# Performance work log

Hardware: AMD Instinct MI355X
Metric: run time of the kernel (lower is better)

The kernel has to match this reference:

```python
import jax, jax.numpy as jnp
import numpy as np

N_EMBD = 1024
NUM_EXPERTS = 8
TOP_K = 2


def new_gelu(x):
    # NewGELU: tanh approximation used by GPT-2
    c = jnp.sqrt(2.0 / jnp.pi).astype(x.dtype)
    return 0.5 * x * (1.0 + jnp.tanh(c * (x + 0.044715 * x ** 3)))


def setup_inputs() -> dict:
    key = jax.random.key(0)
    ks = jax.random.split(key, 6)
    C, E, H = N_EMBD, NUM_EXPERTS, 4 * N_EMBD
    x = jax.random.normal(ks[0], (4, 2048, C), dtype=jnp.float32)
    router_w = 0.02 * jax.random.normal(ks[1], (E, C), dtype=jnp.float32)  # Linear(C,E,bias=False).weight
    w1 = 0.02 * jax.random.normal(ks[2], (E, H, C), dtype=jnp.float32)     # c_fc.weight per expert
    b1 = jnp.zeros((E, H), dtype=jnp.float32)
    w2 = 0.02 * jax.random.normal(ks[3], (E, C, H), dtype=jnp.float32)     # c_proj.weight per expert
    b2 = jnp.zeros((E, C), dtype=jnp.float32)
    return {"x": x, "router_w": router_w, "w1": w1, "b1": b1, "w2": w2, "b2": b2}


def reference(x, router_w, w1, b1, w2, b2):
    B, T, C = x.shape
    E = router_w.shape[0]
    x_flat = x.reshape(B * T, C)  # [N, C]

    router_logits = x_flat @ router_w.T              # [N, E]
    router_probs = jax.nn.softmax(router_logits, axis=-1)
    top_k_probs, top_k_idx = jax.lax.top_k(router_probs, TOP_K)  # [N, K]
    top_k_probs = top_k_probs / (top_k_probs.sum(axis=-1, keepdims=True) + 1e-8)

    # combine weights per (token, expert): sum over k of gate_k * onehot(idx_k)
    cw = (jax.nn.one_hot(top_k_idx, E, dtype=x.dtype) * top_k_probs[..., None]).sum(axis=1)  # [N, E]

    output = jnp.zeros_like(x_flat)
    for e in range(E):  # small fixed expert count
        h = new_gelu(x_flat @ w1[e].T + b1[e])       # [N, 4C]
        out_e = h @ w2[e].T + b2[e]                  # [N, C]
        output = output + cw[:, e:e + 1] * out_e

    return output.reshape(B, T, C)
```

## Files before the change

### kernel.cpp

```cpp
#include <hip/hip_runtime.h>
#include <hip/hip_bf16.h>
#include <math.h>


#define N_TOK   8192
#define C_DIM   1024
#define H_DIM   4096
#define N_EXP   8
#define CAP     8192

typedef __bf16 bf16;
typedef bf16  bf16x8 __attribute__((ext_vector_type(8)));
typedef float f32x4  __attribute__((ext_vector_type(4)));

__device__ __forceinline__ void async_ld16(const void* g, void* l) {
    __builtin_amdgcn_global_load_lds(
        (const __attribute__((address_space(1))) void*)g,
        (__attribute__((address_space(3))) void*)l,
        16, 0, 0);
}

__device__ __forceinline__ float gelu_f(float v) {
    float u = v + 0.044715f * v * v * v;
    return 0.5f * v * (1.0f + tanhf(0.7978845608028654f * u));
}

__global__ void cvt_k(const float* __restrict__ src, bf16* __restrict__ dst, int n8) {
    int i = blockIdx.x * blockDim.x + threadIdx.x;
    if (i >= n8) return;
    const float4* p = (const float4*)src + (size_t)i * 2;
    float4 a = p[0], b = p[1];
    bf16x8 v;
    v[0] = (bf16)a.x; v[1] = (bf16)a.y; v[2] = (bf16)a.z; v[3] = (bf16)a.w;
    v[4] = (bf16)b.x; v[5] = (bf16)b.y; v[6] = (bf16)b.z; v[7] = (bf16)b.w;
    *((bf16x8*)dst + i) = v;
}

__global__ __launch_bounds__(1024) void router_k(const float* __restrict__ x,
                                                 const float* __restrict__ rw,
                                                 int* __restrict__ counts,
                                                 int* __restrict__ tok,
                                                 float* __restrict__ gate) {
    __shared__ int lcnt[N_EXP];
    __shared__ int lbase[N_EXP];
    const int tid  = threadIdx.x;
    const int lane = tid & 63;
    const int wv   = tid >> 6;
    if (tid < N_EXP) lcnt[tid] = 0;
    __syncthreads();

    const int t = blockIdx.x * 16 + wv;

    float dot[N_EXP];
#pragma unroll
    for (int e = 0; e < N_EXP; ++e) dot[e] = 0.f;
    const float4* xr = (const float4*)(x + (size_t)t * C_DIM);
#pragma unroll
    for (int j = 0; j < 4; ++j) {
        float4 xv = xr[j * 64 + lane];
#pragma unroll
        for (int e = 0; e < N_EXP; ++e) {
            float4 w4 = ((const float4*)(rw + (size_t)e * C_DIM))[j * 64 + lane];
            dot[e] += xv.x * w4.x + xv.y * w4.y + xv.z * w4.z + xv.w * w4.w;
        }
    }
#pragma unroll
    for (int e = 0; e < N_EXP; ++e) {
#pragma unroll
        for (int o = 32; o > 0; o >>= 1) dot[e] += __shfl_xor(dot[e], o, 64);
    }

    int a = 0, b = 0, ra = 0, rb = 0;
    float g0 = 0.f, g1 = 0.f;
    if (lane == 0) {
        float m = dot[0];
#pragma unroll
        for (int e = 1; e < N_EXP; ++e) m = fmaxf(m, dot[e]);
        float p[N_EXP]; float s = 0.f;
#pragma unroll
        for (int e = 0; e < N_EXP; ++e) { p[e] = expf(dot[e] - m); s += p[e]; }
        a = 0;
#pragma unroll
        for (int e = 1; e < N_EXP; ++e) if (p[e] > p[a]) a = e;
        b = -1;
#pragma unroll
        for (int e = 0; e < N_EXP; ++e) if (e != a && (b < 0 || p[e] > p[b])) b = e;
        float pa = p[a] / s, pb = p[b] / s;
        float d = pa + pb + 1e-8f;
        g0 = pa / d; g1 = pb / d;
        ra = atomicAdd(&lcnt[a], 1);
        rb = atomicAdd(&lcnt[b], 1);
    }
    __syncthreads();
    if (tid < N_EXP) lbase[tid] = atomicAdd(&counts[tid], lcnt[tid]);
    __syncthreads();
    if (lane == 0) {
        int sa = lbase[a] + ra;
        int sb = lbase[b] + rb;
        tok[a * CAP + sa] = t;  gate[a * CAP + sa] = g0;
        tok[b * CAP + sb] = t;  gate[b * CAP + sb] = g1;
    }
}

__global__ void prefix_k(const int* __restrict__ counts, int* __restrict__ offs) {
    if (threadIdx.x == 0) {
        int s = 0;
        for (int e = 0; e < N_EXP; ++e) { offs[e] = s; s += counts[e]; }
    }
}


__global__ __launch_bounds__(256) void fc1_k(const bf16* __restrict__ xb,
                                             const bf16* __restrict__ w1b,
                                             const float* __restrict__ b1,
                                             const int* __restrict__ counts,
                                             const int* __restrict__ offs,
                                             const int* __restrict__ tok,
                                             bf16* __restrict__ h) {
    const int e   = blockIdx.z;
    const int cnt = counts[e];
    const int m0  = blockIdx.y * 128;
    if (m0 >= cnt) return;
    const int n0  = blockIdx.x * 128;
    const int off = offs[e];

    __shared__ __align__(16) bf16 As[128][32];
    __shared__ __align__(16) bf16 Bs[128][32];

    const int tid  = threadIdx.x;
    const int lane = tid & 63;
    const int wv   = tid >> 6;
    const int wm   = wv & 1;
    const int wn   = wv >> 1;

    const int scol = (((lane & 3) ^ ((lane >> 3) & 3))) * 8;

    const int ar0 = wv * 16 + (lane >> 2);
    const int ar1 = 64 + wv * 16 + (lane >> 2);
    const int i0 = m0 + ar0, i1 = m0 + ar1;
    const int t0 = tok[e * CAP + (i0 < cnt ? i0 : cnt - 1)];
    const int t1 = tok[e * CAP + (i1 < cnt ? i1 : cnt - 1)];
    const bf16* ga0 = xb + (size_t)t0 * C_DIM + scol;
    const bf16* ga1 = xb + (size_t)t1 * C_DIM + scol;
    bf16* la0 = &As[wv * 16][0];
    bf16* la1 = &As[64 + wv * 16][0];

    const bf16* gb0 = w1b + ((size_t)e * H_DIM + n0 + ar0) * C_DIM + scol;
    const bf16* gb1 = w1b + ((size_t)e * H_DIM + n0 + ar1) * C_DIM + scol;
    bf16* lb0 = &Bs[wv * 16][0];
    bf16* lb1 = &Bs[64 + wv * 16][0];

    f32x4 acc[4][4];
#pragma unroll
    for (int mi = 0; mi < 4; ++mi)
#pragma unroll
        for (int ni = 0; ni < 4; ++ni)
#pragma unroll
            for (int r = 0; r < 4; ++r) acc[mi][ni][r] = 0.f;

    const int r_   = lane & 15;
    const int g_   = lane >> 4;
    const int rcol = (g_ ^ ((r_ >> 1) & 3)) * 8;

    for (int kt = 0; kt < C_DIM / 32; ++kt) {
        const int k0 = kt * 32;
        async_ld16(ga0 + k0, la0);
        async_ld16(ga1 + k0, la1);
        async_ld16(gb0 + k0, lb0);
        async_ld16(gb1 + k0, lb1);
        __syncthreads();

        bf16x8 af[4];
#pragma unroll
        for (int mi = 0; mi < 4; ++mi)
            af[mi] = *(const bf16x8*)&As[wm * 64 + mi * 16 + r_][rcol];
#pragma unroll
        for (int ni = 0; ni < 4; ++ni) {
            bf16x8 bfr = *(const bf16x8*)&Bs[wn * 64 + ni * 16 + r_][rcol];
#pragma unroll
            for (int mi = 0; mi < 4; ++mi)
                acc[mi][ni] = __builtin_amdgcn_mfma_f32_16x16x32_bf16(af[mi], bfr, acc[mi][ni], 0, 0, 0);
        }
        __syncthreads();
    }

    const int lg = lane >> 4, ln = lane & 15;
#pragma unroll
    for (int mi = 0; mi < 4; ++mi) {
#pragma unroll
        for (int r = 0; r < 4; ++r) {
            const int m = wm * 64 + mi * 16 + lg * 4 + r;
            if (m0 + m < cnt) {
                const size_t hrow = (size_t)(off + m0 + m) * H_DIM;
#pragma unroll
                for (int ni = 0; ni < 4; ++ni) {
                    const int n = n0 + wn * 64 + ni * 16 + ln;
                    float v = acc[mi][ni][r] + b1[(size_t)e * H_DIM + n];
                    h[hrow + n] = (bf16)gelu_f(v);
                }
            }
        }
    }
}

__global__ __launch_bounds__(256) void fc2_k(const bf16* __restrict__ h,
                                             const bf16* __restrict__ w2b,
                                             const float* __restrict__ b2,
                                             const int* __restrict__ counts,
                                             const int* __restrict__ offs,
                                             const int* __restrict__ tok,
                                             const float* __restrict__ gate,
                                             float* __restrict__ out) {
    const int e   = blockIdx.z;
    const int cnt = counts[e];
    const int m0  = blockIdx.y * 128;
    if (m0 >= cnt) return;
    const int n0  = blockIdx.x * 128;
    const int off = offs[e];

    __shared__ __align__(16) bf16 As[128][32];
    __shared__ __align__(16) bf16 Bs[128][32];

    const int tid  = threadIdx.x;
    const int lane = tid & 63;
    const int wv   = tid >> 6;
    const int wm   = wv & 1;
    const int wn   = wv >> 1;

    const int scol = (((lane & 3) ^ ((lane >> 3) & 3))) * 8;

    const int ar0 = wv * 16 + (lane >> 2);
    const int ar1 = 64 + wv * 16 + (lane >> 2);
    const int i0 = m0 + ar0, i1 = m0 + ar1;
    const size_t hr0 = (size_t)(off + (i0 < cnt ? i0 : cnt - 1)) * H_DIM;
    const size_t hr1 = (size_t)(off + (i1 < cnt ? i1 : cnt - 1)) * H_DIM;
    const bf16* ga0 = h + hr0 + scol;
    const bf16* ga1 = h + hr1 + scol;
    bf16* la0 = &As[wv * 16][0];
    bf16* la1 = &As[64 + wv * 16][0];

    const bf16* gb0 = w2b + ((size_t)e * C_DIM + n0 + ar0) * H_DIM + scol;
    const bf16* gb1 = w2b + ((size_t)e * C_DIM + n0 + ar1) * H_DIM + scol;
    bf16* lb0 = &Bs[wv * 16][0];
    bf16* lb1 = &Bs[64 + wv * 16][0];

    f32x4 acc[4][4];
#pragma unroll
    for (int mi = 0; mi < 4; ++mi)
#pragma unroll
        for (int ni = 0; ni < 4; ++ni)
#pragma unroll
            for (int r = 0; r < 4; ++r) acc[mi][ni][r] = 0.f;

    const int r_   = lane & 15;
    const int g_   = lane >> 4;
    const int rcol = (g_ ^ ((r_ >> 1) & 3)) * 8;

    for (int kt = 0; kt < H_DIM / 32; ++kt) {
        const int k0 = kt * 32;
        async_ld16(ga0 + k0, la0);
        async_ld16(ga1 + k0, la1);
        async_ld16(gb0 + k0, lb0);
        async_ld16(gb1 + k0, lb1);
        __syncthreads();

        bf16x8 af[4];
#pragma unroll
        for (int mi = 0; mi < 4; ++mi)
            af[mi] = *(const bf16x8*)&As[wm * 64 + mi * 16 + r_][rcol];
#pragma unroll
        for (int ni = 0; ni < 4; ++ni) {
            bf16x8 bfr = *(const bf16x8*)&Bs[wn * 64 + ni * 16 + r_][rcol];
#pragma unroll
            for (int mi = 0; mi < 4; ++mi)
                acc[mi][ni] = __builtin_amdgcn_mfma_f32_16x16x32_bf16(af[mi], bfr, acc[mi][ni], 0, 0, 0);
        }
        __syncthreads();
    }

    const int lg = lane >> 4, ln = lane & 15;
#pragma unroll
    for (int mi = 0; mi < 4; ++mi) {
#pragma unroll
        for (int r = 0; r < 4; ++r) {
            const int m = wm * 64 + mi * 16 + lg * 4 + r;
            if (m0 + m < cnt) {
                const int   tk = tok[e * CAP + m0 + m];
                const float g  = gate[e * CAP + m0 + m];
#pragma unroll
                for (int ni = 0; ni < 4; ++ni) {
                    const int n = n0 + wn * 64 + ni * 16 + ln;
                    float v = (acc[mi][ni][r] + b2[(size_t)e * C_DIM + n]) * g;
                    atomicAdd(&out[(size_t)tk * C_DIM + n], v);
                }
            }
        }
    }
}

extern "C" void kernel_launch(void* const* d_in, const int* in_sizes, int n_in,
                              void* d_out, int out_size, void* d_ws, size_t ws_size,
                              hipStream_t stream) {
    const float* x  = (const float*)d_in[0];
    const float* rw = (const float*)d_in[1];
    const float* w1 = (const float*)d_in[2];
    const float* b1 = (const float*)d_in[3];
    const float* w2 = (const float*)d_in[4];
    const float* b2 = (const float*)d_in[5];
    float* out = (float*)d_out;

    char* ws = (char*)d_ws;
    size_t o = 0;
    bf16* xb     = (bf16*)(ws + o);  o += (size_t)N_TOK * C_DIM * sizeof(bf16);
    bf16* w1b    = (bf16*)(ws + o);  o += (size_t)N_EXP * H_DIM * C_DIM * sizeof(bf16);
    bf16* w2b    = (bf16*)(ws + o);  o += (size_t)N_EXP * C_DIM * H_DIM * sizeof(bf16);
    int*  tok    = (int*)(ws + o);   o += (size_t)N_EXP * CAP * sizeof(int);
    float* gate  = (float*)(ws + o); o += (size_t)N_EXP * CAP * sizeof(float);
    int*  counts = (int*)(ws + o);   o += 128;
    int*  offs   = (int*)(ws + o);   o += 128;
    bf16* h      = (bf16*)(ws + o);  o += (size_t)(2 * N_TOK) * H_DIM * sizeof(bf16);

    hipMemsetAsync(d_out, 0, (size_t)N_TOK * C_DIM * sizeof(float), stream);
    hipMemsetAsync(counts, 0, 128, stream);

    const int NW = N_EXP * H_DIM * C_DIM / 8;
    cvt_k<<<dim3((N_TOK * C_DIM / 8 + 255) / 256), 256, 0, stream>>>(x, xb, N_TOK * C_DIM / 8);
    cvt_k<<<dim3((NW + 255) / 256), 256, 0, stream>>>(w1, w1b, NW);
    cvt_k<<<dim3((NW + 255) / 256), 256, 0, stream>>>(w2, w2b, NW);
    router_k<<<dim3(N_TOK / 16), dim3(1024), 0, stream>>>(x, rw, counts, tok, gate);
    prefix_k<<<dim3(1), dim3(64), 0, stream>>>(counts, offs);
    fc1_k<<<dim3(H_DIM / 128, N_TOK / 128, N_EXP), dim3(256), 0, stream>>>(xb, w1b, b1, counts, offs, tok, h);
    fc2_k<<<dim3(C_DIM / 128, N_TOK / 128, N_EXP), dim3(256), 0, stream>>>(h, w2b, b2, counts, offs, tok, gate, out);
}
```

Before: 908.2 us.

## Double-buffer GEMM LDS tiles, remap blocks per XCD, fuse conversions, drop prefix kernel

The fc1 and fc2 GEMM loops now double-buffer the LDS tiles, issuing the async global-to-LDS loads for the next K-step before the MFMAs on the current one, so load latency overlaps compute. Block indices are remapped so consecutive hardware block IDs, which are spread round-robin across the 8 XCDs, map to the same expert's tiles on one XCD, aiming to improve L2 reuse of weights. The three fp32-to-bf16 conversion launches are merged into one kernel, and the prefix-sum kernel is removed by having each GEMM block add up the preceding expert counts itself. Double-buffering doubles LDS per block. Because there is only one barrier per iteration, the next stage's async writes may race with reads of the buffer being overwritten, so it relies on the completion ordering of the async loads.

```diff
diff --git a/kernel.cpp b/kernel.cpp
--- a/kernel.cpp
+++ b/kernel.cpp
@@ -25,15 +25,28 @@
     return 0.5f * v * (1.0f + tanhf(0.7978845608028654f * u));
 }
 
-__global__ void cvt_k(const float* __restrict__ src, bf16* __restrict__ dst, int n8) {
-    int i = blockIdx.x * blockDim.x + threadIdx.x;
-    if (i >= n8) return;
-    const float4* p = (const float4*)src + (size_t)i * 2;
+#define NX8 ((size_t)N_TOK * C_DIM / 8)
+#define NW8 ((size_t)N_EXP * H_DIM * C_DIM / 8)
+#define NCVT (NX8 + 2 * NW8)
+
+__global__ __launch_bounds__(256) void cvt_all_k(const float* __restrict__ x,
+                                                 const float* __restrict__ w1,
+                                                 const float* __restrict__ w2,
+                                                 bf16* __restrict__ xb,
+                                                 bf16* __restrict__ w1b,
+                                                 bf16* __restrict__ w2b) {
+    size_t i = (size_t)blockIdx.x * 256 + threadIdx.x;
+    if (i >= NCVT) return;
+    const float* src; bf16* dst; size_t j;
+    if (i < NX8)            { src = x;  dst = xb;  j = i; }
+    else if (i < NX8 + NW8) { src = w1; dst = w1b; j = i - NX8; }
+    else                    { src = w2; dst = w2b; j = i - NX8 - NW8; }
+    const float4* p = (const float4*)src + j * 2;
     float4 a = p[0], b = p[1];
     bf16x8 v;
     v[0] = (bf16)a.x; v[1] = (bf16)a.y; v[2] = (bf16)a.z; v[3] = (bf16)a.w;
     v[4] = (bf16)b.x; v[5] = (bf16)b.y; v[6] = (bf16)b.z; v[7] = (bf16)b.w;
-    *((bf16x8*)dst + i) = v;
+    *((bf16x8*)dst + j) = v;
 }
 
 __global__ __launch_bounds__(1024) void router_k(const float* __restrict__ x,
@@ -102,30 +115,29 @@
     }
 }
 
-__global__ void prefix_k(const int* __restrict__ counts, int* __restrict__ offs) {
-    if (threadIdx.x == 0) {
-        int s = 0;
-        for (int e = 0; e < N_EXP; ++e) { offs[e] = s; s += counts[e]; }
-    }
-}
-
 
 __global__ __launch_bounds__(256) void fc1_k(const bf16* __restrict__ xb,
                                              const bf16* __restrict__ w1b,
                                              const float* __restrict__ b1,
                                              const int* __restrict__ counts,
-                                             const int* __restrict__ offs,
                                              const int* __restrict__ tok,
                                              bf16* __restrict__ h) {
-    const int e   = blockIdx.z;
+    const int lin = blockIdx.x + 32 * (blockIdx.y + 64 * blockIdx.z);
+    const int w   = (lin & 7) * 2048 + (lin >> 3);
+    const int e   = w >> 11;
+    const int by  = (w >> 5) & 63;
+    const int bx  = w & 31;
+
     const int cnt = counts[e];
-    const int m0  = blockIdx.y * 128;
+    const int m0  = by * 128;
     if (m0 >= cnt) return;
-    const int n0  = blockIdx.x * 128;
-    const int off = offs[e];
-
-    __shared__ __align__(16) bf16 As[128][32];
-    __shared__ __align__(16) bf16 Bs[128][32];
+    const int n0  = bx * 128;
+
+    int off = 0;
+    for (int j = 0; j < e; ++j) off += counts[j];
+
+    __shared__ __align__(16) bf16 As[2][128][32];
+    __shared__ __align__(16) bf16 Bs[2][128][32];
 
     const int tid  = threadIdx.x;
     const int lane = tid & 63;
@@ -136,19 +148,14 @@
     const int scol = (((lane & 3) ^ ((lane >> 3) & 3))) * 8;
 
     const int ar0 = wv * 16 + (lane >> 2);
-    const int ar1 = 64 + wv * 16 + (lane >> 2);
+    const int ar1 = 64 + ar0;
     const int i0 = m0 + ar0, i1 = m0 + ar1;
     const int t0 = tok[e * CAP + (i0 < cnt ? i0 : cnt - 1)];
     const int t1 = tok[e * CAP + (i1 < cnt ? i1 : cnt - 1)];
     const bf16* ga0 = xb + (size_t)t0 * C_DIM + scol;
     const bf16* ga1 = xb + (size_t)t1 * C_DIM + scol;
-    bf16* la0 = &As[wv * 16][0];
-    bf16* la1 = &As[64 + wv * 16][0];
-
     const bf16* gb0 = w1b + ((size_t)e * H_DIM + n0 + ar0) * C_DIM + scol;
     const bf16* gb1 = w1b + ((size_t)e * H_DIM + n0 + ar1) * C_DIM + scol;
-    bf16* lb0 = &Bs[wv * 16][0];
-    bf16* lb1 = &Bs[64 + wv * 16][0];
 
     f32x4 acc[4][4];
 #pragma unroll
@@ -162,27 +169,33 @@
     const int g_   = lane >> 4;
     const int rcol = (g_ ^ ((r_ >> 1) & 3)) * 8;
 
+#define STAGE1(b, kt) do { const int k0_ = (kt) * 32;        \
+    async_ld16(ga0 + k0_, &As[b][wv * 16][0]);               \
+    async_ld16(ga1 + k0_, &As[b][64 + wv * 16][0]);          \
+    async_ld16(gb0 + k0_, &Bs[b][wv * 16][0]);               \
+    async_ld16(gb1 + k0_, &Bs[b][64 + wv * 16][0]); } while (0)
+
+    STAGE1(0, 0);
+    __syncthreads();
+    int cur = 0;
     for (int kt = 0; kt < C_DIM / 32; ++kt) {
-        const int k0 = kt * 32;
-        async_ld16(ga0 + k0, la0);
-        async_ld16(ga1 + k0, la1);
-        async_ld16(gb0 + k0, lb0);
-        async_ld16(gb1 + k0, lb1);
-        __syncthreads();
+        if (kt + 1 < C_DIM / 32) STAGE1(cur ^ 1, kt + 1);
 
         bf16x8 af[4];
 #pragma unroll
         for (int mi = 0; mi < 4; ++mi)
-            af[mi] = *(const bf16x8*)&As[wm * 64 + mi * 16 + r_][rcol];
+            af[mi] = *(const bf16x8*)&As[cur][wm * 64 + mi * 16 + r_][rcol];
 #pragma unroll
         for (int ni = 0; ni < 4; ++ni) {
-            bf16x8 bfr = *(const bf16x8*)&Bs[wn * 64 + ni * 16 + r_][rcol];
+            bf16x8 bfr = *(const bf16x8*)&Bs[cur][wn * 64 + ni * 16 + r_][rcol];
 #pragma unroll
             for (int mi = 0; mi < 4; ++mi)
                 acc[mi][ni] = __builtin_amdgcn_mfma_f32_16x16x32_bf16(af[mi], bfr, acc[mi][ni], 0, 0, 0);
         }
         __syncthreads();
-    }
+        cur ^= 1;
+    }
+#undef STAGE1
 
     const int lg = lane >> 4, ln = lane & 15;
 #pragma unroll
@@ -207,19 +220,25 @@
                                              const bf16* __restrict__ w2b,
                                              const float* __restrict__ b2,
                                              const int* __restrict__ counts,
-                                             const int* __restrict__ offs,
                                              const int* __restrict__ tok,
                                              const float* __restrict__ gate,
                                              float* __restrict__ out) {
-    const int e   = blockIdx.z;
+    const int lin = blockIdx.x + 8 * (blockIdx.y + 64 * blockIdx.z);
+    const int w   = (lin & 7) * 512 + (lin >> 3);
+    const int e   = w >> 9;
+    const int by  = (w >> 3) & 63;
+    const int bx  = w & 7;
+
     const int cnt = counts[e];
-    const int m0  = blockIdx.y * 128;
+    const int m0  = by * 128;
     if (m0 >= cnt) return;
-    const int n0  = blockIdx.x * 128;
-    const int off = offs[e];
-
-    __shared__ __align__(16) bf16 As[128][32];
-    __shared__ __align__(16) bf16 Bs[128][32];
+    const int n0  = bx * 128;
+
+    int off = 0;
+    for (int j = 0; j < e; ++j) off += counts[j];
+
+    __shared__ __align__(16) bf16 As[2][128][32];
+    __shared__ __align__(16) bf16 Bs[2][128][32];
 
     const int tid  = threadIdx.x;
     const int lane = tid & 63;
@@ -230,19 +249,14 @@
     const int scol = (((lane & 3) ^ ((lane >> 3) & 3))) * 8;
 
     const int ar0 = wv * 16 + (lane >> 2);
-    const int ar1 = 64 + wv * 16 + (lane >> 2);
+    const int ar1 = 64 + ar0;
     const int i0 = m0 + ar0, i1 = m0 + ar1;
     const size_t hr0 = (size_t)(off + (i0 < cnt ? i0 : cnt - 1)) * H_DIM;
     const size_t hr1 = (size_t)(off + (i1 < cnt ? i1 : cnt - 1)) * H_DIM;
     const bf16* ga0 = h + hr0 + scol;
     const bf16* ga1 = h + hr1 + scol;
-    bf16* la0 = &As[wv * 16][0];
-    bf16* la1 = &As[64 + wv * 16][0];
-
     const bf16* gb0 = w2b + ((size_t)e * C_DIM + n0 + ar0) * H_DIM + scol;
     const bf16* gb1 = w2b + ((size_t)e * C_DIM + n0 + ar1) * H_DIM + scol;
-    bf16* lb0 = &Bs[wv * 16][0];
-    bf16* lb1 = &Bs[64 + wv * 16][0];
 
     f32x4 acc[4][4];
 #pragma unroll
@@ -256,27 +270,33 @@
     const int g_   = lane >> 4;
     const int rcol = (g_ ^ ((r_ >> 1) & 3)) * 8;
 
+#define STAGE2(b, kt) do { const int k0_ = (kt) * 32;        \
+    async_ld16(ga0 + k0_, &As[b][wv * 16][0]);               \
+    async_ld16(ga1 + k0_, &As[b][64 + wv * 16][0]);          \
+    async_ld16(gb0 + k0_, &Bs[b][wv * 16][0]);               \
+    async_ld16(gb1 + k0_, &Bs[b][64 + wv * 16][0]); } while (0)
+
+    STAGE2(0, 0);
+    __syncthreads();
+    int cur = 0;
     for (int kt = 0; kt < H_DIM / 32; ++kt) {
-        const int k0 = kt * 32;
-        async_ld16(ga0 + k0, la0);
-        async_ld16(ga1 + k0, la1);
-        async_ld16(gb0 + k0, lb0);
-        async_ld16(gb1 + k0, lb1);
-        __syncthreads();
+        if (kt + 1 < H_DIM / 32) STAGE2(cur ^ 1, kt + 1);
 
         bf16x8 af[4];
 #pragma unroll
         for (int mi = 0; mi < 4; ++mi)
-            af[mi] = *(const bf16x8*)&As[wm * 64 + mi * 16 + r_][rcol];
+            af[mi] = *(const bf16x8*)&As[cur][wm * 64 + mi * 16 + r_][rcol];
 #pragma unroll
         for (int ni = 0; ni < 4; ++ni) {
-            bf16x8 bfr = *(const bf16x8*)&Bs[wn * 64 + ni * 16 + r_][rcol];
+            bf16x8 bfr = *(const bf16x8*)&Bs[cur][wn * 64 + ni * 16 + r_][rcol];
 #pragma unroll
             for (int mi = 0; mi < 4; ++mi)
                 acc[mi][ni] = __builtin_amdgcn_mfma_f32_16x16x32_bf16(af[mi], bfr, acc[mi][ni], 0, 0, 0);
         }
         __syncthreads();
-    }
+        cur ^= 1;
+    }
+#undef STAGE2
 
     const int lg = lane >> 4, ln = lane & 15;
 #pragma unroll
@@ -317,18 +337,13 @@
     int*  tok    = (int*)(ws + o);   o += (size_t)N_EXP * CAP * sizeof(int);
     float* gate  = (float*)(ws + o); o += (size_t)N_EXP * CAP * sizeof(float);
     int*  counts = (int*)(ws + o);   o += 128;
-    int*  offs   = (int*)(ws + o);   o += 128;
     bf16* h      = (bf16*)(ws + o);  o += (size_t)(2 * N_TOK) * H_DIM * sizeof(bf16);
 
     hipMemsetAsync(d_out, 0, (size_t)N_TOK * C_DIM * sizeof(float), stream);
     hipMemsetAsync(counts, 0, 128, stream);
 
-    const int NW = N_EXP * H_DIM * C_DIM / 8;
-    cvt_k<<<dim3((N_TOK * C_DIM / 8 + 255) / 256), 256, 0, stream>>>(x, xb, N_TOK * C_DIM / 8);
-    cvt_k<<<dim3((NW + 255) / 256), 256, 0, stream>>>(w1, w1b, NW);
-    cvt_k<<<dim3((NW + 255) / 256), 256, 0, stream>>>(w2, w2b, NW);
+    cvt_all_k<<<dim3((unsigned)((NCVT + 255) / 256)), dim3(256), 0, stream>>>(x, w1, w2, xb, w1b, w2b);
     router_k<<<dim3(N_TOK / 16), dim3(1024), 0, stream>>>(x, rw, counts, tok, gate);
-    prefix_k<<<dim3(1), dim3(64), 0, stream>>>(counts, offs);
-    fc1_k<<<dim3(H_DIM / 128, N_TOK / 128, N_EXP), dim3(256), 0, stream>>>(xb, w1b, b1, counts, offs, tok, h);
-    fc2_k<<<dim3(C_DIM / 128, N_TOK / 128, N_EXP), dim3(256), 0, stream>>>(h, w2b, b2, counts, offs, tok, gate, out);
-}
+    fc1_k<<<dim3(32, 64, N_EXP), dim3(256), 0, stream>>>(xb, w1b, b1, counts, tok, h);
+    fc2_k<<<dim3(8, 64, N_EXP), dim3(256), 0, stream>>>(h, w2b, b2, counts, tok, gate, out);
+}
```

New measurement: 938.9 us. 1.03x slower.
